# Kernel tuning notes

Measured on AMD Instinct MI355X. Metric: run time of the kernel, lower is better.

The kernel has to match this reference:

```python
import jax, jax.numpy as jnp
import numpy as np

B, H, S, D = 2, 16, 2048, 64

def setup_inputs() -> dict:
    key = jax.random.key(0)
    kq, kk, kv = jax.random.split(key, 3)
    q = jax.random.normal(kq, (B, H, S, D), dtype=jnp.float32)
    k = jax.random.normal(kk, (B, H, S, D), dtype=jnp.float32)
    v = jax.random.normal(kv, (B, H, S, D), dtype=jnp.float32)
    # causal mask: True where position j > i (future tokens are masked)
    mask = jnp.triu(jnp.ones((S, S), dtype=bool), k=1)[None, None, :, :]
    return {"q": q, "k": k, "v": v, "mask": mask}

def reference(q, k, v, mask) -> jnp.ndarray:
    # scaled dot-product attention with additive -1e4 mask bias
    scale = 1.0 / jnp.sqrt(jnp.asarray(q.shape[-1], q.dtype))
    scores = jnp.einsum('bhqd,bhkd->bhqk', q, k) * scale  # [B,H,S,S]
    scores = scores + mask.astype(scores.dtype) * jnp.asarray(-10000.0, scores.dtype)
    probs = jax.nn.softmax(scores, axis=-1)
    # dropout is identity in eval mode
    return jnp.einsum('bhqk,bhkd->bhqd', probs, v)
```

## Files before the change

kernel.cpp:

```cpp
#include <hip/hip_runtime.h>

typedef __bf16 bf16_t;
typedef bf16_t bf16x8 __attribute__((ext_vector_type(8)));
typedef bf16_t bf16x4 __attribute__((ext_vector_type(4)));
typedef float  floatx4 __attribute__((ext_vector_type(4)));

constexpr int Sq = 2048, Dq = 64;
constexpr int BQ = 64, BK = 64;
constexpr int NQT = Sq / BQ;
constexpr int STR = 72;
constexpr float SCALE_LOG2E = 0.125f * 1.44269504088896340736f;

__global__ __launch_bounds__(256, 4) void flash_attn_kernel(
    const float* __restrict__ Q, const float* __restrict__ K,
    const float* __restrict__ V, float* __restrict__ O)
{
    __shared__ bf16_t QPs[BQ][STR];
    __shared__ bf16_t Ks[BK][STR];
    __shared__ bf16_t VTs[Dq][STR];

    const int tid  = threadIdx.x;
    const int wave = tid >> 6;
    const int lane = tid & 63;
    const int quad = lane >> 4;
    const int l16  = lane & 15;

    const int id   = blockIdx.x;
    const int g    = id >> 8;
    const int bh   = (id & 7) + (g << 3);
    const int slot = (id >> 3) & 31;
    const int qt   = (g & 1) ? slot : (NQT - 1 - slot);
    const long base = (long)bh * Sq * Dq;

    const int r0 = tid >> 4;
    const int c4 = (tid & 15) * 4;
    const int h  = lane >> 3;
    const int jw = wave * 16;

    #pragma unroll
    for (int p = 0; p < 4; ++p) {
        const int row = p * 16 + r0;
        const float4 qv = *(const float4*)&Q[base + (long)(qt * BQ + row) * Dq + c4];
        bf16x4 w;
        w[0] = (bf16_t)(qv.x * SCALE_LOG2E); w[1] = (bf16_t)(qv.y * SCALE_LOG2E);
        w[2] = (bf16_t)(qv.z * SCALE_LOG2E); w[3] = (bf16_t)(qv.w * SCALE_LOG2E);
        *(bf16x4*)&QPs[row][c4] = w;
    }
    __syncthreads();

    bf16x8 aq0, aq1;
    {
        const int qrow = wave * 16 + l16;
        aq0 = *(const bf16x8*)&QPs[qrow][quad * 8];
        aq1 = *(const bf16x8*)&QPs[qrow][32 + quad * 8];
    }

    float l_lane = 0.f;
    floatx4 o_acc[4];
    #pragma unroll
    for (int i = 0; i < 4; ++i) o_acc[i] = floatx4{0.f, 0.f, 0.f, 0.f};

    float4 kf[4];
    float  vf[4][4];
    #pragma unroll
    for (int p = 0; p < 4; ++p) {
        kf[p] = *(const float4*)&K[base + (long)(p * 16 + r0) * Dq + c4];
        const int j0 = jw + 4 * ((p + h) & 3);
        #pragma unroll
        for (int r = 0; r < 4; ++r)
            vf[p][r] = V[base + (long)(j0 + r) * Dq + lane];
    }

    for (int kt = 0; kt <= qt; ++kt) {
        __syncthreads();

        #pragma unroll
        for (int p = 0; p < 4; ++p) {
            bf16x4 w;
            w[0] = (bf16_t)kf[p].x; w[1] = (bf16_t)kf[p].y;
            w[2] = (bf16_t)kf[p].z; w[3] = (bf16_t)kf[p].w;
            *(bf16x4*)&Ks[p * 16 + r0][c4] = w;
            bf16x4 vw;
            vw[0] = (bf16_t)vf[p][0]; vw[1] = (bf16_t)vf[p][1];
            vw[2] = (bf16_t)vf[p][2]; vw[3] = (bf16_t)vf[p][3];
            *(bf16x4*)&VTs[lane][jw + 4 * ((p + h) & 3)] = vw;
        }
        __syncthreads();

        {
            const int kn = (kt < qt) ? (kt + 1) : qt;
            const long kb = base + (long)kn * BK * Dq;
            #pragma unroll
            for (int p = 0; p < 4; ++p) {
                kf[p] = *(const float4*)&K[kb + (long)(p * 16 + r0) * Dq + c4];
                const int j0 = jw + 4 * ((p + h) & 3);
                #pragma unroll
                for (int r = 0; r < 4; ++r)
                    vf[p][r] = V[kb + (long)(j0 + r) * Dq + lane];
            }
        }

        floatx4 acc[4];
        #pragma unroll
        for (int t = 0; t < 4; ++t) {
            acc[t] = floatx4{0.f, 0.f, 0.f, 0.f};
            const int krow = t * 16 + l16;
            bf16x8 ak0 = *(const bf16x8*)&Ks[krow][quad * 8];
            bf16x8 ak1 = *(const bf16x8*)&Ks[krow][32 + quad * 8];
            acc[t] = __builtin_amdgcn_mfma_f32_16x16x32_bf16(ak0, aq0, acc[t], 0, 0, 0);
            acc[t] = __builtin_amdgcn_mfma_f32_16x16x32_bf16(ak1, aq1, acc[t], 0, 0, 0);
        }

        if (kt == qt) {
            const int qr = wave * 16 + l16;
            #pragma unroll
            for (int t = 0; t < 4; ++t) {
                #pragma unroll
                for (int i = 0; i < 4; ++i) {
                    if (t * 16 + quad * 4 + i > qr) acc[t][i] = -1e30f;
                }
            }
        }

        float l_add = 0.f;
        #pragma unroll
        for (int t = 0; t < 4; ++t) {
            #pragma unroll
            for (int i = 0; i < 4; ++i) {
                acc[t][i] = __builtin_amdgcn_exp2f(acc[t][i]);
                l_add += acc[t][i];
            }
        }
        l_lane += l_add;

        #pragma unroll
        for (int t = 0; t < 4; ++t) {
            bf16x4 pk;
            pk[0] = (bf16_t)acc[t][0]; pk[1] = (bf16_t)acc[t][1];
            pk[2] = (bf16_t)acc[t][2]; pk[3] = (bf16_t)acc[t][3];
            *(bf16x4*)&QPs[wave * 16 + l16][t * 16 + quad * 4] = pk;
        }

        bf16x8 ap0 = *(const bf16x8*)&QPs[wave * 16 + l16][quad * 8];
        bf16x8 ap1 = *(const bf16x8*)&QPs[wave * 16 + l16][32 + quad * 8];
        #pragma unroll
        for (int dt = 0; dt < 4; ++dt) {
            const int dcol = dt * 16 + l16;
            bf16x8 bv0 = *(const bf16x8*)&VTs[dcol][quad * 8];
            bf16x8 bv1 = *(const bf16x8*)&VTs[dcol][32 + quad * 8];
            o_acc[dt] = __builtin_amdgcn_mfma_f32_16x16x32_bf16(ap0, bv0, o_acc[dt], 0, 0, 0);
            o_acc[dt] = __builtin_amdgcn_mfma_f32_16x16x32_bf16(ap1, bv1, o_acc[dt], 0, 0, 0);
        }
    }

    float lsum = l_lane;
    lsum += __shfl_xor(lsum, 16);
    lsum += __shfl_xor(lsum, 32);
    #pragma unroll
    for (int i = 0; i < 4; ++i) {
        const float inv_l = 1.f / __shfl(lsum, quad * 4 + i, 16);
        const long row = (long)qt * BQ + wave * 16 + quad * 4 + i;
        #pragma unroll
        for (int dt = 0; dt < 4; ++dt) {
            O[base + row * Dq + dt * 16 + l16] = o_acc[dt][i] * inv_l;
        }
    }
}

extern "C" void kernel_launch(void* const* d_in, const int* in_sizes, int n_in,
                              void* d_out, int out_size, void* d_ws, size_t ws_size,
                              hipStream_t stream)
{
    const float* q = (const float*)d_in[0];
    const float* k = (const float*)d_in[1];
    const float* v = (const float*)d_in[2];
    float* out = (float*)d_out;
    flash_attn_kernel<<<dim3(1024, 1, 1), dim3(256, 1, 1), 0, stream>>>(q, k, v, out);
}
```

Before: 132.8 us.

## Double-buffer K/V register prefetch two tiles ahead with explicit barriers and setprio

Splits the K/V register prefetch into two alternating buffers so global loads for tile kt+2 are issued while tile kt+1's data is already resident, giving each load more latency-hiding distance. Replaces __syncthreads with raw s_barrier plus sched_barrier and explicit lgkmcnt waits, and raises wave priority around the MFMA blocks. The prefetch now happens after compute rather than before it, and the second register buffer raises VGPR pressure, which could hurt occupancy at 4 blocks per CU.

```diff
diff --git a/kernel.cpp b/kernel.cpp
--- a/kernel.cpp
+++ b/kernel.cpp
@@ -10,6 +10,97 @@
 constexpr int NQT = Sq / BQ;
 constexpr int STR = 72;
 constexpr float SCALE_LOG2E = 0.125f * 1.44269504088896340736f;
+
+#define SBAR() do {                                   \
+    asm volatile("" ::: "memory");                    \
+    __builtin_amdgcn_sched_barrier(0);                \
+    __builtin_amdgcn_s_barrier();                     \
+    __builtin_amdgcn_sched_barrier(0);                \
+    asm volatile("" ::: "memory");                    \
+} while (0)
+
+#define LGKM0() do {                                  \
+    asm volatile("s_waitcnt lgkmcnt(0)" ::: "memory");\
+    __builtin_amdgcn_sched_barrier(0);                \
+} while (0)
+
+#define PREFETCH(kf, vf, kn) do {                                              \
+    const long kb_ = base + (long)(kn) * BK * Dq;                              \
+    _Pragma("unroll")                                                          \
+    for (int p = 0; p < 4; ++p) {                                              \
+        kf[p] = *(const float4*)&K[kb_ + (long)(p * 16 + r0) * Dq + c4];       \
+        const int j0_ = jw + 4 * ((p + h) & 3);                                \
+        _Pragma("unroll")                                                      \
+        for (int r = 0; r < 4; ++r)                                            \
+            vf[p][r] = V[kb_ + (long)(j0_ + r) * Dq + lane];                   \
+    }                                                                          \
+} while (0)
+
+#define STAGE(kf, vf) do {                                                     \
+    _Pragma("unroll")                                                          \
+    for (int p = 0; p < 4; ++p) {                                              \
+        bf16x4 w_;                                                             \
+        w_[0] = (bf16_t)kf[p].x; w_[1] = (bf16_t)kf[p].y;                      \
+        w_[2] = (bf16_t)kf[p].z; w_[3] = (bf16_t)kf[p].w;                      \
+        *(bf16x4*)&Ks[p * 16 + r0][c4] = w_;                                   \
+        bf16x4 vw_;                                                            \
+        vw_[0] = (bf16_t)vf[p][0]; vw_[1] = (bf16_t)vf[p][1];                  \
+        vw_[2] = (bf16_t)vf[p][2]; vw_[3] = (bf16_t)vf[p][3];                  \
+        *(bf16x4*)&VTs[lane][jw + 4 * ((p + h) & 3)] = vw_;                    \
+    }                                                                          \
+} while (0)
+
+#define COMPUTE(DIAG) do {                                                     \
+    floatx4 acc[4];                                                            \
+    __builtin_amdgcn_s_setprio(1);                                             \
+    _Pragma("unroll")                                                          \
+    for (int t = 0; t < 4; ++t) {                                              \
+        acc[t] = floatx4{0.f, 0.f, 0.f, 0.f};                                  \
+        const int krow_ = t * 16 + l16;                                        \
+        bf16x8 ak0 = *(const bf16x8*)&Ks[krow_][quad * 8];                     \
+        bf16x8 ak1 = *(const bf16x8*)&Ks[krow_][32 + quad * 8];                \
+        acc[t] = __builtin_amdgcn_mfma_f32_16x16x32_bf16(ak0, aq0, acc[t], 0, 0, 0); \
+        acc[t] = __builtin_amdgcn_mfma_f32_16x16x32_bf16(ak1, aq1, acc[t], 0, 0, 0); \
+    }                                                                          \
+    __builtin_amdgcn_s_setprio(0);                                             \
+    if (DIAG) {                                                                \
+        const int qr_ = wave * 16 + l16;                                       \
+        _Pragma("unroll")                                                      \
+        for (int t = 0; t < 4; ++t) {                                          \
+            _Pragma("unroll")                                                  \
+            for (int i = 0; i < 4; ++i)                                        \
+                if (t * 16 + quad * 4 + i > qr_) acc[t][i] = -1e30f;           \
+        }                                                                      \
+    }                                                                          \
+    float esum_[4];                                                            \
+    _Pragma("unroll")                                                          \
+    for (int t = 0; t < 4; ++t) {                                              \
+        _Pragma("unroll")                                                      \
+        for (int i = 0; i < 4; ++i)                                            \
+            acc[t][i] = __builtin_amdgcn_exp2f(acc[t][i]);                     \
+        esum_[t] = (acc[t][0] + acc[t][1]) + (acc[t][2] + acc[t][3]);          \
+    }                                                                          \
+    l_lane += (esum_[0] + esum_[1]) + (esum_[2] + esum_[3]);                   \
+    _Pragma("unroll")                                                          \
+    for (int t = 0; t < 4; ++t) {                                              \
+        bf16x4 pk_;                                                            \
+        pk_[0] = (bf16_t)acc[t][0]; pk_[1] = (bf16_t)acc[t][1];                \
+        pk_[2] = (bf16_t)acc[t][2]; pk_[3] = (bf16_t)acc[t][3];                \
+        *(bf16x4*)&QPs[wave * 16 + l16][t * 16 + quad * 4] = pk_;              \
+    }                                                                          \
+    bf16x8 ap0 = *(const bf16x8*)&QPs[wave * 16 + l16][quad * 8];              \
+    bf16x8 ap1 = *(const bf16x8*)&QPs[wave * 16 + l16][32 + quad * 8];         \
+    __builtin_amdgcn_s_setprio(1);                                             \
+    _Pragma("unroll")                                                          \
+    for (int dt = 0; dt < 4; ++dt) {                                           \
+        const int dcol_ = dt * 16 + l16;                                       \
+        bf16x8 bv0 = *(const bf16x8*)&VTs[dcol_][quad * 8];                    \
+        bf16x8 bv1 = *(const bf16x8*)&VTs[dcol_][32 + quad * 8];               \
+        o_acc[dt] = __builtin_amdgcn_mfma_f32_16x16x32_bf16(ap0, bv0, o_acc[dt], 0, 0, 0); \
+        o_acc[dt] = __builtin_amdgcn_mfma_f32_16x16x32_bf16(ap1, bv1, o_acc[dt], 0, 0, 0); \
+    }                                                                          \
+    __builtin_amdgcn_s_setprio(0);                                             \
+} while (0)
 
 __global__ __launch_bounds__(256, 4) void flash_attn_kernel(
     const float* __restrict__ Q, const float* __restrict__ K,
@@ -60,96 +151,26 @@
     #pragma unroll
     for (int i = 0; i < 4; ++i) o_acc[i] = floatx4{0.f, 0.f, 0.f, 0.f};
 
-    float4 kf[4];
-    float  vf[4][4];
-    #pragma unroll
-    for (int p = 0; p < 4; ++p) {
-        kf[p] = *(const float4*)&K[base + (long)(p * 16 + r0) * Dq + c4];
-        const int j0 = jw + 4 * ((p + h) & 3);
-        #pragma unroll
-        for (int r = 0; r < 4; ++r)
-            vf[p][r] = V[base + (long)(j0 + r) * Dq + lane];
-    }
-
-    for (int kt = 0; kt <= qt; ++kt) {
-        __syncthreads();
-
-        #pragma unroll
-        for (int p = 0; p < 4; ++p) {
-            bf16x4 w;
-            w[0] = (bf16_t)kf[p].x; w[1] = (bf16_t)kf[p].y;
-            w[2] = (bf16_t)kf[p].z; w[3] = (bf16_t)kf[p].w;
-            *(bf16x4*)&Ks[p * 16 + r0][c4] = w;
-            bf16x4 vw;
-            vw[0] = (bf16_t)vf[p][0]; vw[1] = (bf16_t)vf[p][1];
-            vw[2] = (bf16_t)vf[p][2]; vw[3] = (bf16_t)vf[p][3];
-            *(bf16x4*)&VTs[lane][jw + 4 * ((p + h) & 3)] = vw;
-        }
-        __syncthreads();
-
-        {
-            const int kn = (kt < qt) ? (kt + 1) : qt;
-            const long kb = base + (long)kn * BK * Dq;
-            #pragma unroll
-            for (int p = 0; p < 4; ++p) {
-                kf[p] = *(const float4*)&K[kb + (long)(p * 16 + r0) * Dq + c4];
-                const int j0 = jw + 4 * ((p + h) & 3);
-                #pragma unroll
-                for (int r = 0; r < 4; ++r)
-                    vf[p][r] = V[kb + (long)(j0 + r) * Dq + lane];
-            }
-        }
-
-        floatx4 acc[4];
-        #pragma unroll
-        for (int t = 0; t < 4; ++t) {
-            acc[t] = floatx4{0.f, 0.f, 0.f, 0.f};
-            const int krow = t * 16 + l16;
-            bf16x8 ak0 = *(const bf16x8*)&Ks[krow][quad * 8];
-            bf16x8 ak1 = *(const bf16x8*)&Ks[krow][32 + quad * 8];
-            acc[t] = __builtin_amdgcn_mfma_f32_16x16x32_bf16(ak0, aq0, acc[t], 0, 0, 0);
-            acc[t] = __builtin_amdgcn_mfma_f32_16x16x32_bf16(ak1, aq1, acc[t], 0, 0, 0);
-        }
-
-        if (kt == qt) {
-            const int qr = wave * 16 + l16;
-            #pragma unroll
-            for (int t = 0; t < 4; ++t) {
-                #pragma unroll
-                for (int i = 0; i < 4; ++i) {
-                    if (t * 16 + quad * 4 + i > qr) acc[t][i] = -1e30f;
-                }
-            }
-        }
-
-        float l_add = 0.f;
-        #pragma unroll
-        for (int t = 0; t < 4; ++t) {
-            #pragma unroll
-            for (int i = 0; i < 4; ++i) {
-                acc[t][i] = __builtin_amdgcn_exp2f(acc[t][i]);
-                l_add += acc[t][i];
-            }
-        }
-        l_lane += l_add;
-
-        #pragma unroll
-        for (int t = 0; t < 4; ++t) {
-            bf16x4 pk;
-            pk[0] = (bf16_t)acc[t][0]; pk[1] = (bf16_t)acc[t][1];
-            pk[2] = (bf16_t)acc[t][2]; pk[3] = (bf16_t)acc[t][3];
-            *(bf16x4*)&QPs[wave * 16 + l16][t * 16 + quad * 4] = pk;
-        }
-
-        bf16x8 ap0 = *(const bf16x8*)&QPs[wave * 16 + l16][quad * 8];
-        bf16x8 ap1 = *(const bf16x8*)&QPs[wave * 16 + l16][32 + quad * 8];
-        #pragma unroll
-        for (int dt = 0; dt < 4; ++dt) {
-            const int dcol = dt * 16 + l16;
-            bf16x8 bv0 = *(const bf16x8*)&VTs[dcol][quad * 8];
-            bf16x8 bv1 = *(const bf16x8*)&VTs[dcol][32 + quad * 8];
-            o_acc[dt] = __builtin_amdgcn_mfma_f32_16x16x32_bf16(ap0, bv0, o_acc[dt], 0, 0, 0);
-            o_acc[dt] = __builtin_amdgcn_mfma_f32_16x16x32_bf16(ap1, bv1, o_acc[dt], 0, 0, 0);
+    float4 kfA[4], kfB[4];
+    float  vfA[4][4], vfB[4][4];
+    PREFETCH(kfA, vfA, 0);
+    PREFETCH(kfB, vfB, (qt > 0 ? 1 : 0));
+
+    for (int kt = 0; kt <= qt; kt += 2) {
+        SBAR();
+        STAGE(kfA, vfA);
+        LGKM0();
+        SBAR();
+        COMPUTE(kt == qt);
+        { const int kn = (kt + 2 <= qt) ? kt + 2 : qt; PREFETCH(kfA, vfA, kn); }
+
+        if (kt + 1 <= qt) {
+            SBAR();
+            STAGE(kfB, vfB);
+            LGKM0();
+            SBAR();
+            COMPUTE(kt + 1 == qt);
+            { const int kn = (kt + 3 <= qt) ? kt + 3 : qt; PREFETCH(kfB, vfB, kn); }
         }
     }
 
```

After: 135.5 us. 2.0% more time.
